# Kernel tuning notes

Measured on AMD Instinct MI355X. Metric: run time of the kernel, lower is better.

Reference implementation:

```python
import jax, jax.numpy as jnp
import numpy as np

S, B, H, K = 2048, 64, 8, 12          # seq_len, input_bits, num_heads, bits per RAM neuron
N_POS = 11                             # bits for relative distance in [0, max_seq_len-1]


def setup_inputs() -> dict:
    key = jax.random.key(0)
    k1, k2, k3, k4, k5 = jax.random.split(key, 5)
    tokens = jax.random.randint(k1, (S, B), 0, 2, dtype=jnp.int32)            # bit tokens
    conn_heads = jax.random.randint(k2, (H, K), 0, 2 * B + N_POS, dtype=jnp.int32)
    head_table = jnp.round(jax.random.uniform(k3, (H, 1 << K))).astype(jnp.float32)  # {0,1} RAM cells
    conn_v = jax.random.randint(k4, (B, K), 0, B, dtype=jnp.int32)
    table_v = jnp.round(jax.random.uniform(k5, (B, 1 << K))).astype(jnp.float32)     # {0,1} RAM cells
    return {"tokens": tokens, "conn_heads": conn_heads, "head_table": head_table,
            "conn_v": conn_v, "table_v": table_v}


def reference(tokens, conn_heads, head_table, conn_v, table_v):
    pow2 = (1 << (K - 1 - jnp.arange(K))).astype(jnp.int32)                 # [K] MSB-first
    tok = tokens.astype(jnp.int32)                                           # [S,B]

    # split each head's 12 connections into query / key / relative-position groups
    grp_q = (conn_heads < B).astype(jnp.int32)
    grp_k = ((conn_heads >= B) & (conn_heads < 2 * B)).astype(jnp.int32)
    grp_p = (conn_heads >= 2 * B).astype(jnp.int32)
    cq = jnp.clip(conn_heads, 0, B - 1)
    ck = jnp.clip(conn_heads - B, 0, B - 1)
    cp = jnp.clip(conn_heads - 2 * B, 0, N_POS - 1)

    # additive address decomposition: addr(i,j,h) = addr_q(i,h)+addr_k(j,h)+addr_p(i-j,h)
    addr_q = (tok[:, cq] * (grp_q * pow2)[None]).sum(-1)                     # [S,H]
    addr_k = (tok[:, ck] * (grp_k * pow2)[None]).sum(-1)                     # [S,H]
    ar = jnp.arange(S)
    posb = ((ar[:, None] >> (N_POS - 1 - jnp.arange(N_POS))[None, :]) & 1).astype(jnp.int32)  # [S,N_POS]
    addr_p = (posb[:, cp] * (grp_p * pow2)[None]).sum(-1)                    # [S,H] indexed by rel dist

    rel = jnp.clip(ar[:, None] - ar[None, :], 0)                             # [S,S]
    addr = addr_q[:, None, :] + addr_k[None, :, :] + addr_p[rel]             # [S,S,H]

    # per-head table lookup, sum over heads = vote counts
    votes = head_table[jnp.arange(H)[None, None, :], addr].sum(-1)           # [S,S]
    causal = ar[None, :] <= ar[:, None]
    votes = jnp.where(causal, votes, 0.0)

    # bit-level value projection: one RAM neuron per output bit
    addr_v = (tok[:, conn_v] * pow2[None, None, :]).sum(-1)                  # [S,B]
    values = table_v[jnp.arange(B)[None, :], addr_v]                         # [S,B]

    # TOP_1 aggregation: first key with max vote; zeros if max vote is 0
    max_vote = votes.max(axis=1)                                             # [S]
    best = jnp.argmax(votes, axis=1)                                         # first occurrence, like the loop
    out = jnp.where((max_vote > 0)[:, None], values[best], 0.0)              # [S,B]
    return out
```

## Files before the change

kernel.cpp:

```cpp
#include <hip/hip_runtime.h>


#define SS 2048
#define BB 64
#define HH 8
#define KK 12
#define NPOS 11
#define TBL 4096
#define TBLW (TBL / 32)


__global__ __launch_bounds__(256) void precompute_kernel(
    const int* __restrict__ tokens,
    const int* __restrict__ conn_heads,
    const float* __restrict__ head_table,
    int* __restrict__ A, int* __restrict__ AK, int* __restrict__ P,
    unsigned int* __restrict__ bits)
{
    int gid = blockIdx.x * blockDim.x + threadIdx.x;
    if (gid < SS * HH) {
        int s = gid >> 3;
        int h = gid & 7;
        int aq = 0, ak = 0, ap = 0;
        #pragma unroll
        for (int k = 0; k < KK; ++k) {
            int c = conn_heads[h * KK + k];
            int sh = KK - 1 - k;
            if (c < BB) {
                aq |= (tokens[s * BB + c] & 1) << sh;
            } else if (c < 2 * BB) {
                ak |= (tokens[s * BB + (c - BB)] & 1) << sh;
            } else {
                int cp = c - 2 * BB;
                ap |= ((s >> (NPOS - 1 - cp)) & 1) << sh;
            }
        }
        A[gid] = aq;
        AK[gid] = ak;
        P[gid] = ap;
    } else {
        int w = gid - SS * HH;
        if (w < HH * TBLW) {
            int h = w >> 7;
            int wi = w & (TBLW - 1);
            unsigned int bv = 0;
            #pragma unroll
            for (int b = 0; b < 32; ++b) {
                if (head_table[h * TBL + wi * 32 + b] > 0.5f) bv |= (1u << b);
            }
            bits[w] = bv;
        }
    }
}

__global__ __launch_bounds__(256) void vote_kernel(
    const int* __restrict__ A, const int* __restrict__ AK, const int* __restrict__ P,
    const unsigned int* __restrict__ bits_g,
    const int* __restrict__ tokens,
    const int* __restrict__ conn_v,
    const float* __restrict__ table_v,
    float* __restrict__ out)
{
    __shared__ unsigned int sbits[HH * TBLW];
    __shared__ int sv[256];
    __shared__ int sj[256];

    const int tid = threadIdx.x;
    const int i = blockIdx.x;

    for (int t = tid; t < HH * TBLW; t += 256) sbits[t] = bits_g[t];
    __syncthreads();

    const int4 a0 = *(const int4*)(A + i * HH);
    const int4 a1 = *(const int4*)(A + i * HH + 4);

    int bv = -1;
    int bj = 0;
    for (int j = tid; j <= i; j += 256) {
        const int4 k0 = *(const int4*)(AK + j * HH);
        const int4 k1 = *(const int4*)(AK + j * HH + 4);
        const int d = i - j;
        const int4 p0 = *(const int4*)(P + d * HH);
        const int4 p1 = *(const int4*)(P + d * HH + 4);
        int v = 0, a;
        a = a0.x | k0.x | p0.x; v += (sbits[(0 << 7) + (a >> 5)] >> (a & 31)) & 1;
        a = a0.y | k0.y | p0.y; v += (sbits[(1 << 7) + (a >> 5)] >> (a & 31)) & 1;
        a = a0.z | k0.z | p0.z; v += (sbits[(2 << 7) + (a >> 5)] >> (a & 31)) & 1;
        a = a0.w | k0.w | p0.w; v += (sbits[(3 << 7) + (a >> 5)] >> (a & 31)) & 1;
        a = a1.x | k1.x | p1.x; v += (sbits[(4 << 7) + (a >> 5)] >> (a & 31)) & 1;
        a = a1.y | k1.y | p1.y; v += (sbits[(5 << 7) + (a >> 5)] >> (a & 31)) & 1;
        a = a1.z | k1.z | p1.z; v += (sbits[(6 << 7) + (a >> 5)] >> (a & 31)) & 1;
        a = a1.w | k1.w | p1.w; v += (sbits[(7 << 7) + (a >> 5)] >> (a & 31)) & 1;
        if (v > bv) { bv = v; bj = j; }
    }

    sv[tid] = bv;
    sj[tid] = bj;
    __syncthreads();
    for (int off = 128; off > 0; off >>= 1) {
        if (tid < off) {
            int v2 = sv[tid + off], j2 = sj[tid + off];
            if (v2 > sv[tid] || (v2 == sv[tid] && j2 < sj[tid])) {
                sv[tid] = v2; sj[tid] = j2;
            }
        }
        __syncthreads();
    }
    const int maxv = sv[0];
    const int best = sj[0];

    if (tid < BB) {
        float o = 0.0f;
        if (maxv > 0) {
            int av = 0;
            #pragma unroll
            for (int k = 0; k < KK; ++k) {
                int c = conn_v[tid * KK + k];
                av |= (tokens[best * BB + c] & 1) << (KK - 1 - k);
            }
            o = table_v[tid * TBL + av];
        }
        out[i * BB + tid] = o;
    }
}

extern "C" void kernel_launch(void* const* d_in, const int* in_sizes, int n_in,
                              void* d_out, int out_size, void* d_ws, size_t ws_size,
                              hipStream_t stream) {
    const int*   tokens     = (const int*)d_in[0];
    const int*   conn_heads = (const int*)d_in[1];
    const float* head_table = (const float*)d_in[2];
    const int*   conn_v     = (const int*)d_in[3];
    const float* table_v    = (const float*)d_in[4];
    float* out = (float*)d_out;

    int* ws = (int*)d_ws;
    int* A  = ws;
    int* AK = ws + SS * HH;
    int* P  = ws + 2 * SS * HH;
    unsigned int* bits = (unsigned int*)(ws + 3 * SS * HH);

    const int total1 = SS * HH + HH * TBLW;
    precompute_kernel<<<(total1 + 255) / 256, 256, 0, stream>>>(
        tokens, conn_heads, head_table, A, AK, P, bits);
    vote_kernel<<<SS, 256, 0, stream>>>(
        A, AK, P, bits, tokens, conn_v, table_v, out);
}
```

Measured before the change: 76.37 us.

## Pair causal rows per block and use packed-key wavefront argmax reduction

Each block now handles row b and row S-1-b, so every block gets the same total causal work and the triangular load is balanced across half as many blocks. The vote and index are packed into one unsigned key (vote in the high bits, inverted index in the low bits), and a wave shuffle max reduces it, replacing the serial shared-memory tree reduction. The bit table is also loaded with a single uint4 per thread. The packing relies on the index fitting in 12 bits and on only 8 heads' worth of votes, and halving the grid reduces the number of blocks available to fill the GPU.

```diff
diff --git a/kernel.cpp b/kernel.cpp
--- a/kernel.cpp
+++ b/kernel.cpp
@@ -8,7 +8,6 @@
 #define NPOS 11
 #define TBL 4096
 #define TBLW (TBL / 32)
-
 
 __global__ __launch_bounds__(256) void precompute_kernel(
     const int* __restrict__ tokens,
@@ -53,6 +52,23 @@
     }
 }
 
+__device__ __forceinline__ int votes8(const unsigned int* sbits,
+                                      const int4& q0, const int4& q1,
+                                      const int4& k0, const int4& k1,
+                                      const int4& p0, const int4& p1)
+{
+    int v = 0, a;
+    a = q0.x | k0.x | p0.x; v += (sbits[0 * TBLW + (a >> 5)] >> (a & 31)) & 1;
+    a = q0.y | k0.y | p0.y; v += (sbits[1 * TBLW + (a >> 5)] >> (a & 31)) & 1;
+    a = q0.z | k0.z | p0.z; v += (sbits[2 * TBLW + (a >> 5)] >> (a & 31)) & 1;
+    a = q0.w | k0.w | p0.w; v += (sbits[3 * TBLW + (a >> 5)] >> (a & 31)) & 1;
+    a = q1.x | k1.x | p1.x; v += (sbits[4 * TBLW + (a >> 5)] >> (a & 31)) & 1;
+    a = q1.y | k1.y | p1.y; v += (sbits[5 * TBLW + (a >> 5)] >> (a & 31)) & 1;
+    a = q1.z | k1.z | p1.z; v += (sbits[6 * TBLW + (a >> 5)] >> (a & 31)) & 1;
+    a = q1.w | k1.w | p1.w; v += (sbits[7 * TBLW + (a >> 5)] >> (a & 31)) & 1;
+    return v;
+}
+
 __global__ __launch_bounds__(256) void vote_kernel(
     const int* __restrict__ A, const int* __restrict__ AK, const int* __restrict__ P,
     const unsigned int* __restrict__ bits_g,
@@ -62,65 +78,76 @@
     float* __restrict__ out)
 {
     __shared__ unsigned int sbits[HH * TBLW];
-    __shared__ int sv[256];
-    __shared__ int sj[256];
+    __shared__ unsigned int skey[2][4];
 
     const int tid = threadIdx.x;
-    const int i = blockIdx.x;
+    const int b = blockIdx.x;
+    const int i0 = b;
+    const int i1 = SS - 1 - b;
 
-    for (int t = tid; t < HH * TBLW; t += 256) sbits[t] = bits_g[t];
+    ((uint4*)sbits)[tid] = ((const uint4*)bits_g)[tid];
     __syncthreads();
 
-    const int4 a0 = *(const int4*)(A + i * HH);
-    const int4 a1 = *(const int4*)(A + i * HH + 4);
+    const int4 q00 = *(const int4*)(A + i0 * HH);
+    const int4 q01 = *(const int4*)(A + i0 * HH + 4);
+    const int4 q10 = *(const int4*)(A + i1 * HH);
+    const int4 q11 = *(const int4*)(A + i1 * HH + 4);
 
-    int bv = -1;
-    int bj = 0;
-    for (int j = tid; j <= i; j += 256) {
+    unsigned int key0 = 0u, key1 = 0u;
+
+    for (int j = tid; j <= i0; j += 256) {
         const int4 k0 = *(const int4*)(AK + j * HH);
         const int4 k1 = *(const int4*)(AK + j * HH + 4);
-        const int d = i - j;
+        const int d = i0 - j;
         const int4 p0 = *(const int4*)(P + d * HH);
         const int4 p1 = *(const int4*)(P + d * HH + 4);
-        int v = 0, a;
-        a = a0.x | k0.x | p0.x; v += (sbits[(0 << 7) + (a >> 5)] >> (a & 31)) & 1;
-        a = a0.y | k0.y | p0.y; v += (sbits[(1 << 7) + (a >> 5)] >> (a & 31)) & 1;
-        a = a0.z | k0.z | p0.z; v += (sbits[(2 << 7) + (a >> 5)] >> (a & 31)) & 1;
-        a = a0.w | k0.w | p0.w; v += (sbits[(3 << 7) + (a >> 5)] >> (a & 31)) & 1;
-        a = a1.x | k1.x | p1.x; v += (sbits[(4 << 7) + (a >> 5)] >> (a & 31)) & 1;
-        a = a1.y | k1.y | p1.y; v += (sbits[(5 << 7) + (a >> 5)] >> (a & 31)) & 1;
-        a = a1.z | k1.z | p1.z; v += (sbits[(6 << 7) + (a >> 5)] >> (a & 31)) & 1;
-        a = a1.w | k1.w | p1.w; v += (sbits[(7 << 7) + (a >> 5)] >> (a & 31)) & 1;
-        if (v > bv) { bv = v; bj = j; }
+        int v = votes8(sbits, q00, q01, k0, k1, p0, p1);
+        unsigned int key = ((unsigned)v << 12) | (unsigned)(4095 - j);
+        key0 = key0 > key ? key0 : key;
+    }
+    for (int j = tid; j <= i1; j += 256) {
+        const int4 k0 = *(const int4*)(AK + j * HH);
+        const int4 k1 = *(const int4*)(AK + j * HH + 4);
+        const int d = i1 - j;
+        const int4 p0 = *(const int4*)(P + d * HH);
+        const int4 p1 = *(const int4*)(P + d * HH + 4);
+        int v = votes8(sbits, q10, q11, k0, k1, p0, p1);
+        unsigned int key = ((unsigned)v << 12) | (unsigned)(4095 - j);
+        key1 = key1 > key ? key1 : key;
     }
 
-    sv[tid] = bv;
-    sj[tid] = bj;
+    #pragma unroll
+    for (int off = 32; off > 0; off >>= 1) {
+        unsigned int o0 = (unsigned int)__shfl_xor((int)key0, off, 64);
+        unsigned int o1 = (unsigned int)__shfl_xor((int)key1, off, 64);
+        key0 = key0 > o0 ? key0 : o0;
+        key1 = key1 > o1 ? key1 : o1;
+    }
+    if ((tid & 63) == 0) {
+        skey[0][tid >> 6] = key0;
+        skey[1][tid >> 6] = key1;
+    }
     __syncthreads();
-    for (int off = 128; off > 0; off >>= 1) {
-        if (tid < off) {
-            int v2 = sv[tid + off], j2 = sj[tid + off];
-            if (v2 > sv[tid] || (v2 == sv[tid] && j2 < sj[tid])) {
-                sv[tid] = v2; sj[tid] = j2;
-            }
-        }
-        __syncthreads();
-    }
-    const int maxv = sv[0];
-    const int best = sj[0];
 
-    if (tid < BB) {
+    if (tid < 128) {
+        const int r = tid >> 6;
+        const int lane = tid & 63;
+        unsigned int ka = skey[r][0] > skey[r][1] ? skey[r][0] : skey[r][1];
+        unsigned int kb = skey[r][2] > skey[r][3] ? skey[r][2] : skey[r][3];
+        unsigned int kf = ka > kb ? ka : kb;
+        const int row = r ? i1 : i0;
         float o = 0.0f;
-        if (maxv > 0) {
+        if ((kf >> 12) > 0) {
+            const int best = 4095 - (int)(kf & 4095u);
             int av = 0;
             #pragma unroll
             for (int k = 0; k < KK; ++k) {
-                int c = conn_v[tid * KK + k];
+                int c = conn_v[lane * KK + k];
                 av |= (tokens[best * BB + c] & 1) << (KK - 1 - k);
             }
-            o = table_v[tid * TBL + av];
+            o = table_v[lane * TBL + av];
         }
-        out[i * BB + tid] = o;
+        out[row * BB + lane] = o;
     }
 }
 
@@ -143,6 +170,6 @@
     const int total1 = SS * HH + HH * TBLW;
     precompute_kernel<<<(total1 + 255) / 256, 256, 0, stream>>>(
         tokens, conn_heads, head_table, A, AK, P, bits);
-    vote_kernel<<<SS, 256, 0, stream>>>(
+    vote_kernel<<<SS / 2, 256, 0, stream>>>(
         A, AK, P, bits, tokens, conn_v, table_v, out);
 }
```

Result: faster. 73.58 us (-3.6%).
